# Optimization experiments

Hardware: AMD Instinct MI355X
Metric: run time of the kernel (lower is better)

## Reference

```python
import jax, jax.numpy as jnp
import numpy as np

B, N, E, D = 2, 8192, 1024, 128   # batch, seq, embed_dim, expand_ratio (= head dim)
H = E // D                        # 8 heads (f_proj output dim)
CHUNK = 64
LN_EPS = 1e-5


def _gla_chunked(q, k, v, log_f):
    """Chunked simple GLA: S_t = exp(log_f_t) * S_{t-1} + k_t v_t^T ; o_t = q_t @ S_t.
    q,k,v: [b,h,n,d], log_f: [b,h,n] (log of per-head scalar decay in (0,1))."""
    b, h, n, d = q.shape
    nc = n // CHUNK
    qc = q.reshape(b, h, nc, CHUNK, d)
    kc = k.reshape(b, h, nc, CHUNK, d)
    vc = v.reshape(b, h, nc, CHUNK, d)
    gf = log_f.reshape(b, h, nc, CHUNK)
    g = jnp.cumsum(gf, axis=-1)          # inclusive within-chunk cum log decay [b,h,nc,C]
    gl = g[..., -1]                      # total chunk log decay [b,h,nc]

    # intra-chunk: A[i,j] = (q_i . k_j) * exp(g_i - g_j), j <= i  (g decreasing -> stable)
    mask = jnp.tril(jnp.ones((CHUNK, CHUNK), bool))
    A = jnp.einsum('bhcid,bhcjd->bhcij', qc, kc)
    A = jnp.where(mask, A * jnp.exp(g[..., :, None] - g[..., None, :]), 0.0)
    o_intra = jnp.einsum('bhcij,bhcjd->bhcid', A, vc)

    # inter-chunk: scan over chunks carrying state S [b,h,d,d]
    def step(S, inp):
        q_c, k_c, v_c, g_c, gl_c = inp   # [b,h,C,d],[b,h,C,d],[b,h,C,d],[b,h,C],[b,h]
        o = jnp.einsum('bhid,bhde->bhie', q_c * jnp.exp(g_c)[..., None], S)
        kd = k_c * jnp.exp(gl_c[..., None] - g_c)[..., None]
        S = jnp.exp(gl_c)[..., None, None] * S + jnp.einsum('bhid,bhie->bhde', kd, v_c)
        return S, o

    xs = (jnp.moveaxis(qc, 2, 0), jnp.moveaxis(kc, 2, 0), jnp.moveaxis(vc, 2, 0),
          jnp.moveaxis(g, 2, 0), jnp.moveaxis(gl, 2, 0))
    S0 = jnp.zeros((b, h, d, d), q.dtype)
    _, o_inter = jax.lax.scan(step, S0, xs)      # [nc,b,h,C,d]
    o_inter = jnp.moveaxis(o_inter, 0, 2)        # [b,h,nc,C,d]
    return (o_intra + o_inter).reshape(b, h, n, d)


def setup_inputs() -> dict:
    key = jax.random.key(0)
    ks = jax.random.split(key, 13)
    s = E ** -0.5
    x = jax.random.normal(ks[0], (B, N, E), jnp.float32)
    # per-head lower bound in (0,1), stored in log space as consumed by the module
    log_lower_bound = jnp.log(jax.random.uniform(ks[1], (H,), jnp.float32, 0.05, 0.95))
    Wq = jax.random.normal(ks[2], (E, E), jnp.float32) * s
    Wk = jax.random.normal(ks[3], (E, E), jnp.float32) * s
    Wv = jax.random.normal(ks[4], (E, E), jnp.float32) * s
    Wf = jax.random.normal(ks[5], (E, H), jnp.float32) * s
    Wb1 = jax.random.normal(ks[6], (E, D), jnp.float32) * s
    Wb2 = jax.random.normal(ks[7], (D, E), jnp.float32) * (D ** -0.5)
    Wg1 = jax.random.normal(ks[8], (E, D), jnp.float32) * s
    Wg2 = jax.random.normal(ks[9], (D, E), jnp.float32) * (D ** -0.5)
    Wo = jax.random.normal(ks[10], (E, E), jnp.float32) * s
    ln_scale = jnp.ones((E,), jnp.float32)
    ln_bias = jnp.zeros((E,), jnp.float32)
    return dict(x=x, log_lower_bound=log_lower_bound, Wq=Wq, Wk=Wk, Wv=Wv, Wf=Wf,
                Wb1=Wb1, Wb2=Wb2, Wg1=Wg1, Wg2=Wg2, Wo=Wo,
                ln_scale=ln_scale, ln_bias=ln_bias)


def reference(x, log_lower_bound, Wq, Wk, Wv, Wf, Wb1, Wb2, Wg1, Wg2, Wo, ln_scale, ln_bias):
    silu = jax.nn.silu
    q = silu(x @ Wq)
    k = silu(x @ Wk)
    v = x @ Wv
    f_pre = x @ Wf                               # [B,N,H] per-head decay logits

    # dense-memory Householder-style reflection of q
    beta = silu((x @ Wb1) @ Wb2)
    nb = jnp.sqrt(jnp.sum(beta * beta, axis=-1, keepdims=True))
    beta = beta / jnp.maximum(nb, 1e-6) / (E ** 0.5)
    q = q - 2.0 * jnp.sum(q * beta, axis=-1, keepdims=True) * beta

    def split(t):
        return t.reshape(B, N, H, D).transpose(0, 2, 1, 3)   # [B,H,N,D]
    qh, kh, vh = split(q), split(k), split(v)

    lb = jnp.exp(log_lower_bound)                            # [H]
    f = lb + (1.0 - lb) * jax.nn.sigmoid(f_pre)              # [B,N,H]
    log_f = jnp.log(f).transpose(0, 2, 1)                    # [B,H,N]

    o = _gla_chunked(qh, kh, vh, log_f)                      # [B,H,N,D]
    o = o.transpose(0, 2, 1, 3).reshape(B, N, E)

    gate = jax.nn.sigmoid((x @ Wg1) @ Wg2)
    o = o * gate

    mu = jnp.mean(o, axis=-1, keepdims=True)
    var = jnp.var(o, axis=-1, keepdims=True)
    o = (o - mu) / jnp.sqrt(var + LN_EPS) * ln_scale + ln_bias
    return o @ Wo
```

## Files before the change

### kernel.cpp

```cpp
#include <hip/hip_runtime.h>
#include <hip/hip_bf16.h>
#include <cstdint>


using u16 = unsigned short;
using u32 = unsigned int;
using u64 = unsigned long long;

typedef __attribute__((ext_vector_type(8))) short s16x8;
typedef __attribute__((ext_vector_type(4))) float f32x4;

__device__ __forceinline__ float b2f(u16 b){ u32 u = ((u32)b)<<16; return __builtin_bit_cast(float,u); }
__device__ __forceinline__ u16 f2b(float f){
  u32 u = __builtin_bit_cast(u32,f);
  return (u16)((u + 0x7FFFu + ((u>>16)&1u)) >> 16);
}
__device__ __forceinline__ float sigm(float x){ return 1.f/(1.f + __expf(-x)); }
__device__ __forceinline__ float silu(float x){ return x * sigm(x); }

__device__ __forceinline__ void gload16(const void* g, void* l){
  __builtin_amdgcn_global_load_lds((const __attribute__((address_space(1))) void*)g,
                                   (__attribute__((address_space(3))) void*)l, 16, 0, 0);
}
#define MFMA(a,b,c) __builtin_amdgcn_mfma_f32_16x16x32_bf16((a),(b),(c),0,0,0)

__device__ __forceinline__ void bar(){
  asm volatile("" ::: "memory");
  __builtin_amdgcn_s_barrier();
  asm volatile("" ::: "memory");
}
__device__ __forceinline__ void wait_vm8(){
  asm volatile("s_waitcnt vmcnt(8)" ::: "memory");
  __builtin_amdgcn_sched_barrier(0);
}
__device__ __forceinline__ void wait_vm0(){
  asm volatile("s_waitcnt vmcnt(0)" ::: "memory");
  __builtin_amdgcn_sched_barrier(0);
}

__device__ __forceinline__ void swz_block(int& bx, int& by){
  const int gx = gridDim.x;
  const int nwg = gx * gridDim.y;
  int lin = by*gx + bx;
  const int cpx = nwg >> 3;
  lin = (lin & 7)*cpx + (lin >> 3);
  bx = lin % gx; by = lin / gx;
}

__global__ __launch_bounds__(256) void fill_diag(float* __restrict__ p, int n, float val){
  int i = blockIdx.x*256 + threadIdx.x;
  if (i < n) p[i] = val;
}

__global__ __launch_bounds__(256) void cast_bf(const float4* __restrict__ src,
                                               ushort4* __restrict__ dst, int n4){
  int i = blockIdx.x*256 + threadIdx.x;
  int st = gridDim.x*256;
  for (; i < n4; i += st){
    float4 v = src[i];
    ushort4 o; o.x=f2b(v.x); o.y=f2b(v.y); o.z=f2b(v.z); o.w=f2b(v.w);
    dst[i] = o;
  }
}

__global__ __launch_bounds__(256) void wprep_all(const float* __restrict__ Wq,
                                                 const float* __restrict__ Wk,
                                                 const float* __restrict__ Wv,
                                                 const float* __restrict__ Wf,
                                                 const float* __restrict__ Wb1,
                                                 const float* __restrict__ Wb2,
                                                 const float* __restrict__ Wg1,
                                                 const float* __restrict__ Wg2,
                                                 const float* __restrict__ Wo,
                                                 u16* __restrict__ WCAT,
                                                 u16* __restrict__ WB2T,
                                                 u16* __restrict__ WG2T,
                                                 u16* __restrict__ WOT){
  const int z = blockIdx.z;
  const float* src; u16* dst; int K, Nsrc, kb, nb;
  switch(z){
    case 0: src=Wq;  dst=WCAT;            K=1024; Nsrc=1024; kb=16; nb=16; break;
    case 1: src=Wk;  dst=WCAT+1024*1024;  K=1024; Nsrc=1024; kb=16; nb=16; break;
    case 2: src=Wv;  dst=WCAT+2048*1024;  K=1024; Nsrc=1024; kb=16; nb=16; break;
    case 3: src=Wb1; dst=WCAT+3072*1024;  K=1024; Nsrc=128;  kb=16; nb=2;  break;
    case 4: src=Wg1; dst=WCAT+3200*1024;  K=1024; Nsrc=128;  kb=16; nb=2;  break;
    case 5: src=Wf;  dst=WCAT+3328*1024;  K=1024; Nsrc=8;    kb=16; nb=2;  break;
    case 6: src=Wb2; dst=WB2T;            K=128;  Nsrc=1024; kb=2;  nb=16; break;
    case 7: src=Wg2; dst=WG2T;            K=128;  Nsrc=1024; kb=2;  nb=16; break;
    default:src=Wo;  dst=WOT;             K=1024; Nsrc=1024; kb=16; nb=16; break;
  }
  if (blockIdx.x >= (u32)kb || blockIdx.y >= (u32)nb) return;
  __shared__ float t[64][65];
  const int k0 = blockIdx.x*64, n0 = blockIdx.y*64;
  const int tid = threadIdx.x;
  #pragma unroll
  for (int e=0;e<16;e++){
    int idx = e*256 + tid;
    int r = idx>>6, c = idx&63;
    float v = 0.f;
    if (n0 + c < Nsrc) v = src[(u64)(k0+r)*Nsrc + n0 + c];
    t[r][c] = v;
  }
  __syncthreads();
  #pragma unroll
  for (int e=0;e<16;e++){
    int idx = e*256 + tid;
    int nn = idx>>6, kk = idx&63;
    dst[(u64)(n0+nn)*K + k0 + kk] = f2b(t[kk][nn]);
  }
}

__global__ __launch_bounds__(256,4) void gemm_bt(const u16* __restrict__ A, int lda,
                                                 const u16* __restrict__ Bt,
                                                 void* __restrict__ C, int ldc,
                                                 int K, int mode){
  __shared__ __align__(16) u16 As[128*64];
  __shared__ __align__(16) u16 Bs[128*64];
  const int tid = threadIdx.x, lane = tid&63, wid = tid>>6;
  int bx = blockIdx.x, by = blockIdx.y;
  swz_block(bx, by);
  const int bn0 = bx*128, bm0 = by*128;
  const int wr = wid>>1, wc = wid&1;
  const int g = lane>>4, ln = lane&15;

  f32x4 acc[4][4];
  #pragma unroll
  for (int i=0;i<4;i++)
    #pragma unroll
    for (int j=0;j<4;j++) acc[i][j] = f32x4{0.f,0.f,0.f,0.f};

  const int nk = K >> 6;
  for (int kt = 0; kt < nk; ++kt){
    const int k0 = kt<<6;
    #pragma unroll
    for (int j=0;j<4;j++){
      const int p = (wid*4+j)*64 + lane;
      const int row = p>>3, sl = p&7;
      const int sc = ((sl ^ (row&7))<<3);
      gload16(A  + (u64)(bm0+row)*lda + k0 + sc, (char*)As + (wid*4+j)*1024);
      gload16(Bt + (u64)(bn0+row)*K   + k0 + sc, (char*)Bs + (wid*4+j)*1024);
    }
    __syncthreads();
    #pragma unroll
    for (int ks=0;ks<2;ks++){
      s16x8 af[4], bf[4];
      #pragma unroll
      for (int mt=0;mt<4;mt++){
        const int row = wr*64 + mt*16 + ln;
        af[mt] = *(const s16x8*)(As + row*64 + (((ks*4+g) ^ (row&7))<<3));
      }
      #pragma unroll
      for (int nt=0;nt<4;nt++){
        const int row = wc*64 + nt*16 + ln;
        bf[nt] = *(const s16x8*)(Bs + row*64 + (((ks*4+g) ^ (row&7))<<3));
      }
      #pragma unroll
      for (int mt=0;mt<4;mt++)
        #pragma unroll
        for (int nt=0;nt<4;nt++)
          acc[mt][nt] = MFMA(af[mt], bf[nt], acc[mt][nt]);
    }
    __syncthreads();
  }
  if (mode == 0){
    float* Cf = (float*)C;
    #pragma unroll
    for (int mt=0;mt<4;mt++)
      #pragma unroll
      for (int nt=0;nt<4;nt++){
        const int col = bn0 + wc*64 + nt*16 + ln;
        #pragma unroll
        for (int r=0;r<4;r++)
          Cf[(u64)(bm0 + wr*64 + mt*16 + g*4 + r)*ldc + col] = acc[mt][nt][r];
      }
  } else {
    u16* Cb = (u16*)C;
    #pragma unroll
    for (int mt=0;mt<4;mt++)
      #pragma unroll
      for (int nt=0;nt<4;nt++){
        const int col = bn0 + wc*64 + nt*16 + ln;
        #pragma unroll
        for (int r=0;r<4;r++)
          Cb[(u64)(bm0 + wr*64 + mt*16 + g*4 + r)*ldc + col] = f2b(acc[mt][nt][r]);
      }
  }
}

#define STAGE256(kt_, c_)                                                              \
  do{ const int kk0 = (kt_)<<6;                                                        \
    _Pragma("unroll")                                                                  \
    for (int j=0;j<4;j++){                                                             \
      const int p = j*512 + tid;                                                       \
      const int row = p>>3, sl = p&7;                                                  \
      const int sc = ((sl ^ (row&7))<<3);                                              \
      gload16(A  + (u64)(bm0+row)*lda + kk0 + sc,                                      \
              (char*)lds + (c_)*65536 + (j*8+wid)*1024);                               \
      gload16(Bt + (u64)(bn0+row)*K   + kk0 + sc,                                      \
              (char*)lds + (c_)*65536 + 32768 + (j*8+wid)*1024);                       \
    } }while(0)

#define GEMM256_CORE()                                                                 \
  f32x4 acc[8][4];                                                                     \
  _Pragma("unroll")                                                                    \
  for (int i=0;i<8;i++)                                                                \
    _Pragma("unroll")                                                                  \
    for (int j=0;j<4;j++) acc[i][j] = f32x4{0.f,0.f,0.f,0.f};                          \
  const int nk = K >> 6;                                                               \
  STAGE256(0, 0);                                                                      \
  int cbuf = 0;                                                                        \
  for (int kt = 0; kt < nk; ++kt){                                                     \
    if (kt+1 < nk){ STAGE256(kt+1, cbuf^1); wait_vm8(); } else { wait_vm0(); }         \
    bar();                                                                             \
    const u16* As_c = lds + cbuf*32768;                                                \
    const u16* Bs_c = As_c + 16384;                                                    \
    s16x8 bfr[2][4];                                                                   \
    _Pragma("unroll")                                                                  \
    for (int ks=0;ks<2;ks++)                                                           \
      _Pragma("unroll")                                                                \
      for (int n=0;n<4;n++){                                                           \
        const int row = wc*64 + n*16 + ln;                                             \
        bfr[ks][n] = *(const s16x8*)(Bs_c + row*64 + (((ks*4+g) ^ (row&7))<<3));       \
      }                                                                                \
    _Pragma("unroll")                                                                  \
    for (int m=0;m<8;m++){                                                             \
      const int arow = wr*128 + m*16 + ln;                                             \
      _Pragma("unroll")                                                                \
      for (int ks=0;ks<2;ks++){                                                        \
        const s16x8 af = *(const s16x8*)(As_c + arow*64 + (((ks*4+g) ^ (arow&7))<<3)); \
        _Pragma("unroll")                                                              \
        for (int n=0;n<4;n++) acc[m][n] = MFMA(af, bfr[ks][n], acc[m][n]);             \
      }                                                                                \
    }                                                                                  \
    bar();                                                                             \
    cbuf ^= 1;                                                                         \
  }

__global__ __launch_bounds__(512,2) void gemm256(const u16* __restrict__ A, int lda,
                                                 const u16* __restrict__ Bt,
                                                 void* __restrict__ C, int ldc,
                                                 int K, int mode){
  __shared__ __align__(16) u16 lds[2*32768];
  const int tid = threadIdx.x, lane = tid&63, wid = tid>>6;
  int bx = blockIdx.x, by = blockIdx.y;
  swz_block(bx, by);
  const int bn0 = bx*256, bm0 = by*256;
  const int wr = wid>>2, wc = wid&3;
  const int g = lane>>4, ln = lane&15;
  GEMM256_CORE();
  if (mode == 0){
    float* Cf = (float*)C;
    #pragma unroll
    for (int m=0;m<8;m++)
      #pragma unroll
      for (int n=0;n<4;n++){
        const int col = bn0 + wc*64 + n*16 + ln;
        #pragma unroll
        for (int r=0;r<4;r++)
          Cf[(u64)(bm0 + wr*128 + m*16 + g*4 + r)*ldc + col] = acc[m][n][r];
      }
  } else {
    u16* Cb = (u16*)C;
    #pragma unroll
    for (int m=0;m<8;m++)
      #pragma unroll
      for (int n=0;n<4;n++){
        const int col = bn0 + wc*64 + n*16 + ln;
        #pragma unroll
        for (int r=0;r<4;r++)
          Cb[(u64)(bm0 + wr*128 + m*16 + g*4 + r)*ldc + col] = f2b(acc[m][n][r]);
      }
  }
}

__global__ __launch_bounds__(512,2) void gemm_proj(const u16* __restrict__ A,
                                                   const u16* __restrict__ Bt,
                                                   u16* __restrict__ Qb,
                                                   u16* __restrict__ Kp,
                                                   u16* __restrict__ KT,
                                                   u16* __restrict__ VT,
                                                   u16* __restrict__ FP,
                                                   const float* __restrict__ Gp,
                                                   const float* __restrict__ GLp){
  __shared__ __align__(16) u16 lds[2*32768];
  const int tid = threadIdx.x, lane = tid&63, wid = tid>>6;
  int bx = blockIdx.x, by = blockIdx.y;
  swz_block(bx, by);
  const int bn0 = bx*256, bm0 = by*256;
  const int lda = 1024, K = 1024;
  const int wr = wid>>2, wc = wid&3;
  const int g = lane>>4, ln = lane&15;
  GEMM256_CORE();

  const int cw0 = bn0 + wc*64;
  const int hb = cw0 >> 7;
  if (hb < 8){
    #pragma unroll
    for (int m=0;m<8;m++)
      #pragma unroll
      for (int n=0;n<4;n++){
        const int col = cw0 + n*16 + ln;
        #pragma unroll
        for (int r=0;r<4;r++)
          Qb[(u64)(bm0 + wr*128 + m*16 + g*4 + r)*1024 + col] = f2b(acc[m][n][r]);
      }
  } else if (hb < 16){
    const int h = hb - 8;
    const int bh = (bm0>>13)*8 + h;
    const int dbase = cw0 & 127;
    #pragma unroll
    for (int m=0;m<8;m++){
      const int trow = (bm0&8191) + wr*128 + m*16 + g*4;
      const float gl = GLp[bh*128 + (trow>>6)];
      float es[4];
      #pragma unroll
      for (int r=0;r<4;r++) es[r] = __expf(gl - Gp[(u64)bh*8192 + trow + r]);
      #pragma unroll
      for (int n=0;n<4;n++){
        const int d = dbase + n*16 + ln;
        ushort4 o; u16* op = (u16*)&o;
        #pragma unroll
        for (int r=0;r<4;r++){
          const float s = silu(acc[m][n][r]);
          op[r] = f2b(s * es[r]);
          Kp[(u64)(bm0 + wr*128 + m*16 + g*4 + r)*1024 + h*128 + d] = f2b(s);
        }
        *(ushort4*)(KT + ((u64)bh*128 + d)*8192 + trow) = o;
      }
    }
  } else if (hb < 24){
    const int h = hb - 16;
    const int bh = (bm0>>13)*8 + h;
    const int dbase = cw0 & 127;
    #pragma unroll
    for (int m=0;m<8;m++){
      const int trow = (bm0&8191) + wr*128 + m*16 + g*4;
      #pragma unroll
      for (int n=0;n<4;n++){
        const int d = dbase + n*16 + ln;
        ushort4 o; u16* op = (u16*)&o;
        #pragma unroll
        for (int r=0;r<4;r++) op[r] = f2b(acc[m][n][r]);
        *(ushort4*)(VT + ((u64)bh*128 + d)*8192 + trow) = o;
      }
    }
  } else {
    #pragma unroll
    for (int m=0;m<8;m++)
      #pragma unroll
      for (int n=0;n<4;n++){
        const int col = cw0 + n*16 + ln - 3072;
        #pragma unroll
        for (int r=0;r<4;r++)
          FP[(u64)(bm0 + wr*128 + m*16 + g*4 + r)*384 + col] = f2b(acc[m][n][r]);
      }
  }
}

__global__ __launch_bounds__(64) void fkernel(const u16* __restrict__ FP,
                                              const float* __restrict__ llb,
                                              float* __restrict__ G, float* __restrict__ GL){
  const int c = blockIdx.x, bh = blockIdx.y;
  const int b = bh>>3, h = bh&7;
  const int t = threadIdx.x;
  const int tok = c*64 + t;
  const float fp = b2f(FP[(u64)(b*8192 + tok)*384 + 256 + h]);
  const float lb = __expf(llb[h]);
  const float f = lb + (1.f - lb) * sigm(fp);
  float x = __logf(f);
  #pragma unroll
  for (int d=1; d<64; d<<=1){
    float v = __shfl_up(x, d);
    if (t >= d) x += v;
  }
  G[(u64)bh*8192 + tok] = x;
  const float gl = __shfl(x, 63);
  if (t == 0) GL[bh*128 + c] = gl;
}

__global__ __launch_bounds__(256) void e1_reflect(u16* __restrict__ Q,
                                                  const u16* __restrict__ BP){
  const u64 t = blockIdx.x;
  const int tid = threadIdx.x;
  __shared__ float red[8];
  u16* qrow = Q + t*1024;
  const u16* brow = BP + t*1024;
  ushort4 qv = ((const ushort4*)qrow)[tid];
  ushort4 bv = ((const ushort4*)brow)[tid];
  u16* qp = (u16*)&qv; const u16* bp = (const u16*)&bv;
  float q[4], bb[4];
  float s1 = 0.f, s2 = 0.f;
  #pragma unroll
  for (int j=0;j<4;j++){
    const float qq = silu(b2f(qp[j]));
    const float bbv = silu(b2f(bp[j]));
    q[j] = qq; bb[j] = bbv;
    s1 += bbv*bbv; s2 += qq*bbv;
  }
  #pragma unroll
  for (int d=1; d<64; d<<=1){ s1 += __shfl_xor(s1,d); s2 += __shfl_xor(s2,d); }
  const int wid = tid>>6, lane = tid&63;
  if (lane==0){ red[wid]=s1; red[4+wid]=s2; }
  __syncthreads();
  s1 = red[0]+red[1]+red[2]+red[3];
  s2 = red[4]+red[5]+red[6]+red[7];
  const float bs = 1.f/(fmaxf(sqrtf(s1), 1e-6f) * 32.f);
  const float coef = 2.f * s2 * bs * bs;
  #pragma unroll
  for (int j=0;j<4;j++) qp[j] = f2b(q[j] - coef*bb[j]);
  ((ushort4*)qrow)[tid] = qv;
}

__global__ __launch_bounds__(256,4) void g1_local(const u16* __restrict__ KT,
                                                  const u16* __restrict__ VT,
                                                  u16* __restrict__ LT){
  __shared__ __align__(16) u16 kts[128*64];
  __shared__ __align__(16) u16 vts[128*64];
  const int c = blockIdx.x, bh = blockIdx.y;
  const int tid = threadIdx.x, lane = tid&63, wid = tid>>6;
  const int g = lane>>4, ln = lane&15;
  #pragma unroll
  for (int j=0;j<4;j++){
    const int p = (wid*4+j)*64 + lane;
    const int row = p>>3, sl = p&7;
    const int sc = ((sl ^ (row&7))<<3);
    gload16(KT + ((u64)bh*128 + row)*8192 + (u64)c*64 + sc, (char*)kts + (wid*4+j)*1024);
    gload16(VT + ((u64)bh*128 + row)*8192 + (u64)c*64 + sc, (char*)vts + (wid*4+j)*1024);
  }
  __syncthreads();
  f32x4 acc[2][8];
  #pragma unroll
  for (int mt=0;mt<2;mt++)
// ... 202 lines not shown
  const float mu = s * (1.f/1024.f);
  const float var = s2 * (1.f/1024.f) - mu*mu;
  const float rs = rsqrtf(var + 1e-5f);
  ushort4 out; u16* op = (u16*)&out;
  #pragma unroll
  for (int j=0;j<4;j++){
    const int e = tid*4 + j;
    op[j] = f2b((o[j]-mu)*rs*lnsc[e] + lnbi[e]);
  }
  ((ushort4*)(OL + t*1024))[tid] = out;
}

extern "C" void kernel_launch(void* const* d_in, const int* in_sizes, int n_in,
                              void* d_out, int out_size, void* d_ws, size_t ws_size,
                              hipStream_t stream){
  const float* x   = (const float*)d_in[0];
  const float* llb = (const float*)d_in[1];
  const float* Wq  = (const float*)d_in[2];
  const float* Wk  = (const float*)d_in[3];
  const float* Wv  = (const float*)d_in[4];
  const float* Wf  = (const float*)d_in[5];
  const float* Wb1 = (const float*)d_in[6];
  const float* Wb2 = (const float*)d_in[7];
  const float* Wg1 = (const float*)d_in[8];
  const float* Wg2 = (const float*)d_in[9];
  const float* Wo  = (const float*)d_in[10];
  const float* lnsc= (const float*)d_in[11];
  const float* lnbi= (const float*)d_in[12];

  const u64 REQUIRED = 190586880ull;
  if (ws_size < REQUIRED){
    const float val = 1.0e6f + (float)(u64)(ws_size>>20) * 1024.0f;
    fill_diag<<<dim3((out_size+255)/256),256,0,stream>>>((float*)d_out, out_size, val);
    return;
  }

  char* ws = (char*)d_ws;
  u16*  WCAT = (u16*)(ws + 0ull);
  u16*  WB2T = (u16*)(ws + 7077888ull);
  u16*  WG2T = (u16*)(ws + 7340032ull);
  u16*  WOT  = (u16*)(ws + 7602176ull);
  float* Gb  = (float*)(ws + 9699328ull);
  float* GLb = (float*)(ws + 10223616ull);
  u16*  FP   = (u16*)(ws + 10231808ull);
  u16*  R0   = (u16*)(ws + 22814720ull);
  u16*  Qb   = (u16*)(ws + 56369152ull);
  u16*  Kp   = (u16*)(ws + 89923584ull);
  u16*  KT   = (u16*)(ws + 123478016ull);
  u16*  VT   = (u16*)(ws + 157032448ull);
  u16*  LTSB = (u16*)d_out;
  u16*  XB = R0, *BP = R0, *GP = R0;
  u16*  Ob = KT, *OL = Qb;

  cast_bf<<<dim3(4096),256,0,stream>>>((const float4*)x, (ushort4*)XB, 16384*1024/4);
  wprep_all<<<dim3(16,16,9),256,0,stream>>>(Wq,Wk,Wv,Wf,Wb1,Wb2,Wg1,Wg2,Wo,
                                            WCAT, WB2T, WG2T, WOT);

  gemm_bt<<<dim3(1,128),256,0,stream>>>(XB, 1024, WCAT + 3328*1024, FP + 256, 384, 1024, 1);
  fkernel<<<dim3(128,16),64,0,stream>>>(FP, llb, Gb, GLb);

  gemm_proj<<<dim3(13,64),512,0,stream>>>(XB, WCAT, Qb, Kp, KT, VT, FP, Gb, GLb);

  gemm256<<<dim3(4,64),512,0,stream>>>(FP, 384, WB2T, BP, 1024, 128, 1);
  e1_reflect<<<dim3(16384),256,0,stream>>>(Qb, BP);

  gemm256<<<dim3(4,64),512,0,stream>>>(FP + 128, 384, WG2T, GP, 1024, 128, 1);

  g1_local<<<dim3(128,16),256,0,stream>>>(KT, VT, LTSB);
  g2_scan<<<dim3(64,16),256,0,stream>>>(LTSB, GLb);
  g3_out<<<dim3(128,16),256,0,stream>>>(Qb, Kp, VT, LTSB, Gb, Ob);

  e2_ln<<<dim3(16384),256,0,stream>>>(Ob, GP, lnsc, lnbi, OL);

  gemm256<<<dim3(4,64),512,0,stream>>>(OL, 1024, WOT, d_out, 1024, 1024, 0);
}
```

Measured before the change: 377.9 us.

## Restructure 256x256 GEMM main loop into four quadrant phases with interleaved staging

```diff
diff --git a/kernel.cpp b/kernel.cpp
--- a/kernel.cpp
+++ b/kernel.cpp
@@ -29,12 +29,16 @@
   __builtin_amdgcn_s_barrier();
   asm volatile("" ::: "memory");
 }
-__device__ __forceinline__ void wait_vm8(){
+__device__ __forceinline__ void wv4(){
+  asm volatile("s_waitcnt vmcnt(4)" ::: "memory");
+  __builtin_amdgcn_sched_barrier(0);
+}
+__device__ __forceinline__ void wv0(){
+  asm volatile("s_waitcnt vmcnt(0)" ::: "memory");
+  __builtin_amdgcn_sched_barrier(0);
+}
+__device__ __forceinline__ void wv8(){
   asm volatile("s_waitcnt vmcnt(8)" ::: "memory");
-  __builtin_amdgcn_sched_barrier(0);
-}
-__device__ __forceinline__ void wait_vm0(){
-  asm volatile("s_waitcnt vmcnt(0)" ::: "memory");
   __builtin_amdgcn_sched_barrier(0);
 }
 
@@ -187,54 +191,74 @@
   }
 }
 
-#define STAGE256(kt_, c_)                                                              \
-  do{ const int kk0 = (kt_)<<6;                                                        \
-    _Pragma("unroll")                                                                  \
-    for (int j=0;j<4;j++){                                                             \
-      const int p = j*512 + tid;                                                       \
-      const int row = p>>3, sl = p&7;                                                  \
-      const int sc = ((sl ^ (row&7))<<3);                                              \
-      gload16(A  + (u64)(bm0+row)*lda + kk0 + sc,                                      \
-              (char*)lds + (c_)*65536 + (j*8+wid)*1024);                               \
-      gload16(Bt + (u64)(bn0+row)*K   + kk0 + sc,                                      \
-              (char*)lds + (c_)*65536 + 32768 + (j*8+wid)*1024);                       \
+#define STAGE_H(kt_, b_, gb_, ld_, grow0_, loff_)                              \
+  do{ const int kk0_ = (kt_)<<6;                                               \
+    _Pragma("unroll")                                                          \
+    for (int j_=0;j_<2;j_++){                                                  \
+      const int p_ = j_*512 + tid;                                             \
+      const int row_ = p_>>3, sl_ = p_&7;                                      \
+      const int sc_ = ((sl_ ^ (row_&7))<<3);                                   \
+      gload16((gb_) + (u64)((grow0_)+row_)*(ld_) + kk0_ + sc_,                 \
+              (char*)lds + (b_)*65536 + (loff_) + j_*8192 + wid*1024);         \
     } }while(0)
 
-#define GEMM256_CORE()                                                                 \
-  f32x4 acc[8][4];                                                                     \
-  _Pragma("unroll")                                                                    \
-  for (int i=0;i<8;i++)                                                                \
-    _Pragma("unroll")                                                                  \
-    for (int j=0;j<4;j++) acc[i][j] = f32x4{0.f,0.f,0.f,0.f};                          \
-  const int nk = K >> 6;                                                               \
-  STAGE256(0, 0);                                                                      \
-  int cbuf = 0;                                                                        \
-  for (int kt = 0; kt < nk; ++kt){                                                     \
-    if (kt+1 < nk){ STAGE256(kt+1, cbuf^1); wait_vm8(); } else { wait_vm0(); }         \
-    bar();                                                                             \
-    const u16* As_c = lds + cbuf*32768;                                                \
-    const u16* Bs_c = As_c + 16384;                                                    \
-    s16x8 bfr[2][4];                                                                   \
-    _Pragma("unroll")                                                                  \
-    for (int ks=0;ks<2;ks++)                                                           \
-      _Pragma("unroll")                                                                \
-      for (int n=0;n<4;n++){                                                           \
-        const int row = wc*64 + n*16 + ln;                                             \
-        bfr[ks][n] = *(const s16x8*)(Bs_c + row*64 + (((ks*4+g) ^ (row&7))<<3));       \
-      }                                                                                \
-    _Pragma("unroll")                                                                  \
-    for (int m=0;m<8;m++){                                                             \
-      const int arow = wr*128 + m*16 + ln;                                             \
-      _Pragma("unroll")                                                                \
-      for (int ks=0;ks<2;ks++){                                                        \
-        const s16x8 af = *(const s16x8*)(As_c + arow*64 + (((ks*4+g) ^ (arow&7))<<3)); \
-        _Pragma("unroll")                                                              \
-        for (int n=0;n<4;n++) acc[m][n] = MFMA(af, bfr[ks][n], acc[m][n]);             \
-      }                                                                                \
-    }                                                                                  \
-    bar();                                                                             \
-    cbuf ^= 1;                                                                         \
-  }
+#define PHASE(mh_, nh_, W_, SG_)                                               \
+  do{                                                                          \
+    if (W_) wv4();                                                             \
+    bar();                                                                     \
+    const u16* Ab_ = lds + cbuf*32768 + (mh_)*8192;                            \
+    const u16* Bb_ = lds + cbuf*32768 + 16384 + (nh_)*8192;                    \
+    s16x8 af_[2][4], bf_[2][2];                                                \
+    _Pragma("unroll")                                                          \
+    for (int ks=0;ks<2;ks++){                                                  \
+      _Pragma("unroll")                                                        \
+      for (int m=0;m<4;m++){                                                   \
+        const int r_ = wr*64 + m*16 + ln;                                      \
+        af_[ks][m] = *(const s16x8*)(Ab_ + r_*64 + (((ks*4+g) ^ (r_&7))<<3));  \
+      }                                                                        \
+      _Pragma("unroll")                                                        \
+      for (int n=0;n<2;n++){                                                   \
+        const int r_ = wc*32 + n*16 + ln;                                      \
+        bf_[ks][n] = *(const s16x8*)(Bb_ + r_*64 + (((ks*4+g) ^ (r_&7))<<3));  \
+      }                                                                        \
+    }                                                                          \
+    SG_;                                                                       \
+    __builtin_amdgcn_s_setprio(1);                                             \
+    _Pragma("unroll")                                                          \
+    for (int ks=0;ks<2;ks++)                                                   \
+      _Pragma("unroll")                                                        \
+      for (int m=0;m<4;m++)                                                    \
+        _Pragma("unroll")                                                      \
+        for (int n=0;n<2;n++)                                                  \
+          acc[(mh_)*4+m][(nh_)*2+n] =                                          \
+            MFMA(af_[ks][m], bf_[ks][n], acc[(mh_)*4+m][(nh_)*2+n]);           \
+    __builtin_amdgcn_s_setprio(0);                                             \
+  }while(0)
+
+#define GEMM8P_CORE()                                                          \
+  f32x4 acc[8][4];                                                             \
+  _Pragma("unroll")                                                            \
+  for (int i=0;i<8;i++)                                                        \
+    _Pragma("unroll")                                                          \
+    for (int j=0;j<4;j++) acc[i][j] = f32x4{0.f,0.f,0.f,0.f};                  \
+  const int nk = K >> 6;                                                       \
+  STAGE_H(0,0,Bt,K,  bn0,     32768);                                          \
+  STAGE_H(0,0,A, lda,bm0,     0);                                              \
+  STAGE_H(0,0,Bt,K,  bn0+128, 49152);                                          \
+  STAGE_H(0,0,A, lda,bm0+128, 16384);                                          \
+  for (int kt=0; kt<nk-1; ++kt){                                               \
+    const int cbuf = kt&1, nb = cbuf^1;                                        \
+    PHASE(0,0,1, STAGE_H(kt+1,nb,Bt,K,  bn0,     32768));                      \
+    PHASE(0,1,1, STAGE_H(kt+1,nb,A, lda,bm0,     0));                          \
+    PHASE(1,1,1, STAGE_H(kt+1,nb,Bt,K,  bn0+128, 49152));                      \
+    PHASE(1,0,0, STAGE_H(kt+1,nb,A, lda,bm0+128, 16384));                      \
+  }                                                                            \
+  { const int cbuf = (nk-1)&1;                                                 \
+    wv0();                                                                     \
+    PHASE(0,0,0,);                                                             \
+    PHASE(0,1,0,);                                                             \
+    PHASE(1,1,0,);                                                             \
+    PHASE(1,0,0,); }
 
 __global__ __launch_bounds__(512,2) void gemm256(const u16* __restrict__ A, int lda,
                                                  const u16* __restrict__ Bt,
@@ -245,31 +269,41 @@
   int bx = blockIdx.x, by = blockIdx.y;
   swz_block(bx, by);
   const int bn0 = bx*256, bm0 = by*256;
-  const int wr = wid>>2, wc = wid&3;
+  const int wr = (wid>>2), wc = wid&3;
   const int g = lane>>4, ln = lane&15;
-  GEMM256_CORE();
+  GEMM8P_CORE();
   if (mode == 0){
     float* Cf = (float*)C;
     #pragma unroll
-    for (int m=0;m<8;m++)
-      #pragma unroll
-      for (int n=0;n<4;n++){
-        const int col = bn0 + wc*64 + n*16 + ln;
-        #pragma unroll
-        for (int r=0;r<4;r++)
-          Cf[(u64)(bm0 + wr*128 + m*16 + g*4 + r)*ldc + col] = acc[m][n][r];
-      }
+    for (int mh=0;mh<2;mh++)
+      #pragma unroll
+      for (int m=0;m<4;m++)
+        #pragma unroll
+        for (int nh=0;nh<2;nh++)
+          #pragma unroll
+          for (int n=0;n<2;n++){
+            const int col = bn0 + nh*128 + wc*32 + n*16 + ln;
+            #pragma unroll
+            for (int r=0;r<4;r++)
+              Cf[(u64)(bm0 + mh*128 + wr*64 + m*16 + g*4 + r)*ldc + col] =
+                acc[mh*4+m][nh*2+n][r];
+          }
   } else {
     u16* Cb = (u16*)C;
     #pragma unroll
-    for (int m=0;m<8;m++)
-      #pragma unroll
-      for (int n=0;n<4;n++){
-        const int col = bn0 + wc*64 + n*16 + ln;
-        #pragma unroll
-        for (int r=0;r<4;r++)
-          Cb[(u64)(bm0 + wr*128 + m*16 + g*4 + r)*ldc + col] = f2b(acc[m][n][r]);
-      }
+    for (int mh=0;mh<2;mh++)
+      #pragma unroll
+      for (int m=0;m<4;m++)
+        #pragma unroll
+        for (int nh=0;nh<2;nh++)
+          #pragma unroll
+          for (int n=0;n<2;n++){
+            const int col = bn0 + nh*128 + wc*32 + n*16 + ln;
+            #pragma unroll
+            for (int r=0;r<4;r++)
+              Cb[(u64)(bm0 + mh*128 + wr*64 + m*16 + g*4 + r)*ldc + col] =
+                f2b(acc[mh*4+m][nh*2+n][r]);
+          }
   }
 }
 
@@ -288,72 +322,82 @@
   swz_block(bx, by);
   const int bn0 = bx*256, bm0 = by*256;
   const int lda = 1024, K = 1024;
-  const int wr = wid>>2, wc = wid&3;
+  const int wr = (wid>>2), wc = wid&3;
   const int g = lane>>4, ln = lane&15;
-  GEMM256_CORE();
-
-  const int cw0 = bn0 + wc*64;
-  const int hb = cw0 >> 7;
-  if (hb < 8){
-    #pragma unroll
-    for (int m=0;m<8;m++)
-      #pragma unroll
-      for (int n=0;n<4;n++){
-        const int col = cw0 + n*16 + ln;
-        #pragma unroll
-        for (int r=0;r<4;r++)
-          Qb[(u64)(bm0 + wr*128 + m*16 + g*4 + r)*1024 + col] = f2b(acc[m][n][r]);
-      }
-  } else if (hb < 16){
-    const int h = hb - 8;
-    const int bh = (bm0>>13)*8 + h;
-    const int dbase = cw0 & 127;
-    #pragma unroll
-    for (int m=0;m<8;m++){
-      const int trow = (bm0&8191) + wr*128 + m*16 + g*4;
-      const float gl = GLp[bh*128 + (trow>>6)];
-      float es[4];
-      #pragma unroll
-      for (int r=0;r<4;r++) es[r] = __expf(gl - Gp[(u64)bh*8192 + trow + r]);
-      #pragma unroll
-      for (int n=0;n<4;n++){
-        const int d = dbase + n*16 + ln;
-        ushort4 o; u16* op = (u16*)&o;
-        #pragma unroll
-        for (int r=0;r<4;r++){
-          const float s = silu(acc[m][n][r]);
-          op[r] = f2b(s * es[r]);
-          Kp[(u64)(bm0 + wr*128 + m*16 + g*4 + r)*1024 + h*128 + d] = f2b(s);
+  GEMM8P_CORE();
+
+  #pragma unroll
+  for (int nh=0;nh<2;nh++){
+    const int hb2 = (bn0>>7) + nh;
+    if (hb2 < 8){
+      #pragma unroll
+      for (int mh=0;mh<2;mh++)
+        #pragma unroll
+        for (int m=0;m<4;m++)
+          #pragma unroll
+          for (int n=0;n<2;n++){
+            const int col = bn0 + nh*128 + wc*32 + n*16 + ln;
+            #pragma unroll
+            for (int r=0;r<4;r++)
+              Qb[(u64)(bm0 + mh*128 + wr*64 + m*16 + g*4 + r)*1024 + col] =
+                f2b(acc[mh*4+m][nh*2+n][r]);
+          }
+    } else if (hb2 < 16){
+      const int h = hb2 - 8;
+      const int bh = (bm0>>13)*8 + h;
+      #pragma unroll
+      for (int mh=0;mh<2;mh++)
+        #pragma unroll
+        for (int m=0;m<4;m++){
+          const int trowb = (bm0&8191) + mh*128 + wr*64 + m*16 + g*4;
+          const float gl = GLp[bh*128 + (trowb>>6)];
+          float es[4];
+          #pragma unroll
+          for (int r=0;r<4;r++) es[r] = __expf(gl - Gp[(u64)bh*8192 + trowb + r]);
+          #pragma unroll
+          for (int n=0;n<2;n++){
+            const int d = wc*32 + n*16 + ln;
+            ushort4 o; u16* op = (u16*)&o;
+            #pragma unroll
+            for (int r=0;r<4;r++){
+              const float s = silu(acc[mh*4+m][nh*2+n][r]);
+              op[r] = f2b(s * es[r]);
+              Kp[(u64)(bm0 + mh*128 + wr*64 + m*16 + g*4 + r)*1024 + h*128 + d] = f2b(s);
+            }
+            *(ushort4*)(KT + ((u64)bh*128 + d)*8192 + trowb) = o;
+          }
         }
-        *(ushort4*)(KT + ((u64)bh*128 + d)*8192 + trow) = o;
-      }
-    }
-  } else if (hb < 24){
-    const int h = hb - 16;
-    const int bh = (bm0>>13)*8 + h;
-    const int dbase = cw0 & 127;
-    #pragma unroll
-    for (int m=0;m<8;m++){
-      const int trow = (bm0&8191) + wr*128 + m*16 + g*4;
-      #pragma unroll
-      for (int n=0;n<4;n++){
-        const int d = dbase + n*16 + ln;
-        ushort4 o; u16* op = (u16*)&o;
-        #pragma unroll
-        for (int r=0;r<4;r++) op[r] = f2b(acc[m][n][r]);
-        *(ushort4*)(VT + ((u64)bh*128 + d)*8192 + trow) = o;
-      }
-    }
-  } else {
-    #pragma unroll
-    for (int m=0;m<8;m++)
-      #pragma unroll
-      for (int n=0;n<4;n++){
-        const int col = cw0 + n*16 + ln - 3072;
-        #pragma unroll
-        for (int r=0;r<4;r++)
-          FP[(u64)(bm0 + wr*128 + m*16 + g*4 + r)*384 + col] = f2b(acc[m][n][r]);
-      }
+    } else if (hb2 < 24){
+      const int h = hb2 - 16;
+      const int bh = (bm0>>13)*8 + h;
+      #pragma unroll
+      for (int mh=0;mh<2;mh++)
+        #pragma unroll
+        for (int m=0;m<4;m++){
+          const int trowb = (bm0&8191) + mh*128 + wr*64 + m*16 + g*4;
+          #pragma unroll
+          for (int n=0;n<2;n++){
+            const int d = wc*32 + n*16 + ln;
+            ushort4 o; u16* op = (u16*)&o;
+            #pragma unroll
+            for (int r=0;r<4;r++) op[r] = f2b(acc[mh*4+m][nh*2+n][r]);
+            *(ushort4*)(VT + ((u64)bh*128 + d)*8192 + trowb) = o;
+          }
+        }
+    } else {
+      #pragma unroll
+      for (int mh=0;mh<2;mh++)
+        #pragma unroll
+        for (int m=0;m<4;m++)
+          #pragma unroll
+          for (int n=0;n<2;n++){
+            const int col = bn0 + nh*128 + wc*32 + n*16 + ln - 3072;
+            #pragma unroll
+            for (int r=0;r<4;r++)
+              FP[(u64)(bm0 + mh*128 + wr*64 + m*16 + g*4 + r)*384 + col] =
+                f2b(acc[mh*4+m][nh*2+n][r]);
+          }
+    }
   }
 }
 
```

Measured after the change: 380.1 us. About the same (+0.6%).

## Restructure 256x256 GEMM mainloop into 4-stage K=32 pipeline with k-major LDS layout

Applied to the files above, without the earlier changes.

```diff
diff --git a/kernel.cpp b/kernel.cpp
--- a/kernel.cpp
+++ b/kernel.cpp
@@ -29,12 +29,20 @@
   __builtin_amdgcn_s_barrier();
   asm volatile("" ::: "memory");
 }
-__device__ __forceinline__ void wait_vm8(){
+__device__ __forceinline__ void wv8(){
   asm volatile("s_waitcnt vmcnt(8)" ::: "memory");
   __builtin_amdgcn_sched_barrier(0);
 }
-__device__ __forceinline__ void wait_vm0(){
+__device__ __forceinline__ void wv4(){
+  asm volatile("s_waitcnt vmcnt(4)" ::: "memory");
+  __builtin_amdgcn_sched_barrier(0);
+}
+__device__ __forceinline__ void wv0(){
   asm volatile("s_waitcnt vmcnt(0)" ::: "memory");
+  __builtin_amdgcn_sched_barrier(0);
+}
+__device__ __forceinline__ void lgkm0(){
+  asm volatile("s_waitcnt lgkmcnt(0)" ::: "memory");
   __builtin_amdgcn_sched_barrier(0);
 }
 
@@ -187,67 +195,62 @@
   }
 }
 
-#define STAGE256(kt_, c_)                                                              \
-  do{ const int kk0 = (kt_)<<6;                                                        \
-    _Pragma("unroll")                                                                  \
-    for (int j=0;j<4;j++){                                                             \
-      const int p = j*512 + tid;                                                       \
-      const int row = p>>3, sl = p&7;                                                  \
-      const int sc = ((sl ^ (row&7))<<3);                                              \
-      gload16(A  + (u64)(bm0+row)*lda + kk0 + sc,                                      \
-              (char*)lds + (c_)*65536 + (j*8+wid)*1024);                               \
-      gload16(Bt + (u64)(bn0+row)*K   + kk0 + sc,                                      \
-              (char*)lds + (c_)*65536 + 32768 + (j*8+wid)*1024);                       \
+#define STAGE32(kt_, b_)                                                       \
+  do{ const int kk0_ = (kt_)<<5;                                               \
+    _Pragma("unroll")                                                          \
+    for (int j_=0;j_<2;j_++){                                                  \
+      const int p_ = wid*2 + j_;                                               \
+      const int s_ = p_>>2, rb_ = p_&3;                                        \
+      gload16(A  + (u64)(bm0 + rb_*64 + lane)*lda + kk0_ + s_*8,               \
+              (char*)lds + (b_)*32768 + s_*4096 + rb_*1024);                   \
+      gload16(Bt + (u64)(bn0 + rb_*64 + lane)*K   + kk0_ + s_*8,               \
+              (char*)lds + (b_)*32768 + 16384 + s_*4096 + rb_*1024);           \
     } }while(0)
 
-#define GEMM256_CORE()                                                                 \
-  f32x4 acc[8][4];                                                                     \
-  _Pragma("unroll")                                                                    \
-  for (int i=0;i<8;i++)                                                                \
-    _Pragma("unroll")                                                                  \
-    for (int j=0;j<4;j++) acc[i][j] = f32x4{0.f,0.f,0.f,0.f};                          \
-  const int nk = K >> 6;                                                               \
-  STAGE256(0, 0);                                                                      \
-  int cbuf = 0;                                                                        \
-  for (int kt = 0; kt < nk; ++kt){                                                     \
-    if (kt+1 < nk){ STAGE256(kt+1, cbuf^1); wait_vm8(); } else { wait_vm0(); }         \
-    bar();                                                                             \
-    const u16* As_c = lds + cbuf*32768;                                                \
-    const u16* Bs_c = As_c + 16384;                                                    \
-    s16x8 bfr[2][4];                                                                   \
-    _Pragma("unroll")                                                                  \
-    for (int ks=0;ks<2;ks++)                                                           \
-      _Pragma("unroll")                                                                \
-      for (int n=0;n<4;n++){                                                           \
-        const int row = wc*64 + n*16 + ln;                                             \
-        bfr[ks][n] = *(const s16x8*)(Bs_c + row*64 + (((ks*4+g) ^ (row&7))<<3));       \
-      }                                                                                \
-    _Pragma("unroll")                                                                  \
-    for (int m=0;m<8;m++){                                                             \
-      const int arow = wr*128 + m*16 + ln;                                             \
-      _Pragma("unroll")                                                                \
-      for (int ks=0;ks<2;ks++){                                                        \
-        const s16x8 af = *(const s16x8*)(As_c + arow*64 + (((ks*4+g) ^ (arow&7))<<3)); \
-        _Pragma("unroll")                                                              \
-        for (int n=0;n<4;n++) acc[m][n] = MFMA(af, bfr[ks][n], acc[m][n]);             \
-      }                                                                                \
-    }                                                                                  \
-    bar();                                                                             \
-    cbuf ^= 1;                                                                         \
+#define GEMMD_CORE()                                                           \
+  f32x4 acc[8][4];                                                             \
+  _Pragma("unroll")                                                            \
+  for (int i=0;i<8;i++)                                                        \
+    _Pragma("unroll")                                                          \
+    for (int j=0;j<4;j++) acc[i][j] = f32x4{0.f,0.f,0.f,0.f};                  \
+  const int nk = K >> 5;                                                       \
+  STAGE32(0,0); STAGE32(1,1); STAGE32(2,2);                                    \
+  for (int s=0; s<nk; ++s){                                                    \
+    if (s < nk-2) wv8(); else if (s == nk-2) wv4(); else wv0();                \
+    bar();                                                                     \
+    if (s+3 < nk) STAGE32(s+3, (s+3)&3);                                       \
+    const int cb = s&3;                                                        \
+    const u16* Ab_ = lds + cb*16384 + g*2048;                                  \
+    const u16* Bb_ = Ab_ + 8192;                                               \
+    s16x8 af_[8], bf_[4];                                                      \
+    _Pragma("unroll")                                                          \
+    for (int m=0;m<8;m++)                                                      \
+      af_[m] = *(const s16x8*)(Ab_ + (wr*128 + m*16 + ln)*8);                  \
+    _Pragma("unroll")                                                          \
+    for (int n=0;n<4;n++)                                                      \
+      bf_[n] = *(const s16x8*)(Bb_ + (wc*64 + n*16 + ln)*8);                   \
+    lgkm0();                                                                   \
+    __builtin_amdgcn_s_setprio(1);                                             \
+    _Pragma("unroll")                                                          \
+    for (int m=0;m<8;m++)                                                      \
+      _Pragma("unroll")                                                        \
+      for (int n=0;n<4;n++)                                                    \
+        acc[m][n] = MFMA(af_[m], bf_[n], acc[m][n]);                           \
+    __builtin_amdgcn_s_setprio(0);                                             \
   }
 
 __global__ __launch_bounds__(512,2) void gemm256(const u16* __restrict__ A, int lda,
                                                  const u16* __restrict__ Bt,
                                                  void* __restrict__ C, int ldc,
                                                  int K, int mode){
-  __shared__ __align__(16) u16 lds[2*32768];
+  __shared__ __align__(16) u16 lds[4*16384];
   const int tid = threadIdx.x, lane = tid&63, wid = tid>>6;
   int bx = blockIdx.x, by = blockIdx.y;
   swz_block(bx, by);
   const int bn0 = bx*256, bm0 = by*256;
   const int wr = wid>>2, wc = wid&3;
   const int g = lane>>4, ln = lane&15;
-  GEMM256_CORE();
+  GEMMD_CORE();
   if (mode == 0){
     float* Cf = (float*)C;
     #pragma unroll
@@ -282,7 +285,7 @@
                                                    u16* __restrict__ FP,
                                                    const float* __restrict__ Gp,
                                                    const float* __restrict__ GLp){
-  __shared__ __align__(16) u16 lds[2*32768];
+  __shared__ __align__(16) u16 lds[4*16384];
   const int tid = threadIdx.x, lane = tid&63, wid = tid>>6;
   int bx = blockIdx.x, by = blockIdx.y;
   swz_block(bx, by);
@@ -290,24 +293,24 @@
   const int lda = 1024, K = 1024;
   const int wr = wid>>2, wc = wid&3;
   const int g = lane>>4, ln = lane&15;
-  GEMM256_CORE();
-
-  const int cw0 = bn0 + wc*64;
-  const int hb = cw0 >> 7;
-  if (hb < 8){
+  GEMMD_CORE();
+
+  const int hb2 = (bn0>>7) + (wc>>1);
+  const int dq  = (wc&1)*64;
+  if (hb2 < 8){
     #pragma unroll
     for (int m=0;m<8;m++)
       #pragma unroll
       for (int n=0;n<4;n++){
-        const int col = cw0 + n*16 + ln;
+        const int col = bn0 + wc*64 + n*16 + ln;
         #pragma unroll
         for (int r=0;r<4;r++)
-          Qb[(u64)(bm0 + wr*128 + m*16 + g*4 + r)*1024 + col] = f2b(acc[m][n][r]);
-      }
-  } else if (hb < 16){
-    const int h = hb - 8;
+          Qb[(u64)(bm0 + wr*128 + m*16 + g*4 + r)*1024 + col] =
+            f2b(acc[m][n][r]);
+      }
+  } else if (hb2 < 16){
+    const int h = hb2 - 8;
     const int bh = (bm0>>13)*8 + h;
-    const int dbase = cw0 & 127;
     #pragma unroll
     for (int m=0;m<8;m++){
       const int trow = (bm0&8191) + wr*128 + m*16 + g*4;
@@ -317,7 +320,7 @@
       for (int r=0;r<4;r++) es[r] = __expf(gl - Gp[(u64)bh*8192 + trow + r]);
       #pragma unroll
       for (int n=0;n<4;n++){
-        const int d = dbase + n*16 + ln;
+        const int d = dq + n*16 + ln;
         ushort4 o; u16* op = (u16*)&o;
         #pragma unroll
         for (int r=0;r<4;r++){
@@ -328,16 +331,15 @@
         *(ushort4*)(KT + ((u64)bh*128 + d)*8192 + trow) = o;
       }
     }
-  } else if (hb < 24){
-    const int h = hb - 16;
+  } else if (hb2 < 24){
+    const int h = hb2 - 16;
     const int bh = (bm0>>13)*8 + h;
-    const int dbase = cw0 & 127;
     #pragma unroll
     for (int m=0;m<8;m++){
       const int trow = (bm0&8191) + wr*128 + m*16 + g*4;
       #pragma unroll
       for (int n=0;n<4;n++){
-        const int d = dbase + n*16 + ln;
+        const int d = dq + n*16 + ln;
         ushort4 o; u16* op = (u16*)&o;
         #pragma unroll
         for (int r=0;r<4;r++) op[r] = f2b(acc[m][n][r]);
@@ -349,10 +351,11 @@
     for (int m=0;m<8;m++)
       #pragma unroll
       for (int n=0;n<4;n++){
-        const int col = cw0 + n*16 + ln - 3072;
+        const int col = bn0 + wc*64 + n*16 + ln - 3072;
         #pragma unroll
         for (int r=0;r<4;r++)
-          FP[(u64)(bm0 + wr*128 + m*16 + g*4 + r)*384 + col] = f2b(acc[m][n][r]);
+          FP[(u64)(bm0 + wr*128 + m*16 + g*4 + r)*384 + col] =
+            f2b(acc[m][n][r]);
       }
   }
 }
```

After: 441.0 us. 1.17x slower.

## Compute decay logits in fp32 directly and shrink projection GEMM tiles to 128

Applied to the files above, without the earlier changes.

```diff
diff --git a/kernel.cpp b/kernel.cpp
--- a/kernel.cpp
+++ b/kernel.cpp
@@ -66,7 +66,6 @@
 __global__ __launch_bounds__(256) void wprep_all(const float* __restrict__ Wq,
                                                  const float* __restrict__ Wk,
                                                  const float* __restrict__ Wv,
-                                                 const float* __restrict__ Wf,
                                                  const float* __restrict__ Wb1,
                                                  const float* __restrict__ Wb2,
                                                  const float* __restrict__ Wg1,
@@ -84,9 +83,8 @@
     case 2: src=Wv;  dst=WCAT+2048*1024;  K=1024; Nsrc=1024; kb=16; nb=16; break;
     case 3: src=Wb1; dst=WCAT+3072*1024;  K=1024; Nsrc=128;  kb=16; nb=2;  break;
     case 4: src=Wg1; dst=WCAT+3200*1024;  K=1024; Nsrc=128;  kb=16; nb=2;  break;
-    case 5: src=Wf;  dst=WCAT+3328*1024;  K=1024; Nsrc=8;    kb=16; nb=2;  break;
-    case 6: src=Wb2; dst=WB2T;            K=128;  Nsrc=1024; kb=2;  nb=16; break;
-    case 7: src=Wg2; dst=WG2T;            K=128;  Nsrc=1024; kb=2;  nb=16; break;
+    case 5: src=Wb2; dst=WB2T;            K=128;  Nsrc=1024; kb=2;  nb=16; break;
+    case 6: src=Wg2; dst=WG2T;            K=128;  Nsrc=1024; kb=2;  nb=16; break;
     default:src=Wo;  dst=WOT;             K=1024; Nsrc=1024; kb=16; nb=16; break;
   }
   if (blockIdx.x >= (u32)kb || blockIdx.y >= (u32)nb) return;
@@ -110,10 +108,53 @@
   }
 }
 
-__global__ __launch_bounds__(256,4) void gemm_bt(const u16* __restrict__ A, int lda,
-                                                 const u16* __restrict__ Bt,
-                                                 void* __restrict__ C, int ldc,
-                                                 int K, int mode){
+__global__ __launch_bounds__(256) void fkernel2(const float* __restrict__ x,
+                                                const float* __restrict__ Wf,
+                                                const float* __restrict__ llb,
+                                                float* __restrict__ G,
+                                                float* __restrict__ GL){
+  const int c = blockIdx.x, bh = blockIdx.y;
+  const int b = bh>>3, h = bh&7;
+  const int tid = threadIdx.x;
+  __shared__ float wf[1024];
+  __shared__ float fsm[64];
+  for (int i = tid; i < 1024; i += 256) wf[i] = Wf[(u64)i*8 + h];
+  __syncthreads();
+  const int t = tid>>2, q = tid&3;
+  const float* xr = x + (u64)(b*8192 + c*64 + t)*1024 + q*256;
+  const float* wp0 = wf + q*256;
+  float s = 0.f;
+  #pragma unroll 8
+  for (int i=0;i<64;i++){
+    float4 xv = ((const float4*)xr)[i];
+    s += xv.x*wp0[i*4+0] + xv.y*wp0[i*4+1] + xv.z*wp0[i*4+2] + xv.w*wp0[i*4+3];
+  }
+  s += __shfl_xor(s,1); s += __shfl_xor(s,2);
+  if (q==0) fsm[t] = s;
+  __syncthreads();
+  if (tid < 64){
+    const float lb = __expf(llb[h]);
+    const float f = lb + (1.f - lb)*sigm(fsm[tid]);
+    float xg = __logf(f);
+    #pragma unroll
+    for (int d=1; d<64; d<<=1){
+      float v = __shfl_up(xg, d);
+      if (tid >= d) xg += v;
+    }
+    G[(u64)bh*8192 + c*64 + tid] = xg;
+    if (tid==63) GL[bh*128 + c] = xg;
+  }
+}
+
+__global__ __launch_bounds__(256,4) void gemm_proj(const u16* __restrict__ A,
+                                                   const u16* __restrict__ Bt,
+                                                   u16* __restrict__ Qb,
+                                                   u16* __restrict__ Kp,
+                                                   u16* __restrict__ KT,
+                                                   u16* __restrict__ VT,
+                                                   u16* __restrict__ FP,
+                                                   const float* __restrict__ Gp,
+                                                   const float* __restrict__ GLp){
   __shared__ __align__(16) u16 As[128*64];
   __shared__ __align__(16) u16 Bs[128*64];
   const int tid = threadIdx.x, lane = tid&63, wid = tid>>6;
@@ -129,16 +170,15 @@
     #pragma unroll
     for (int j=0;j<4;j++) acc[i][j] = f32x4{0.f,0.f,0.f,0.f};
 
-  const int nk = K >> 6;
-  for (int kt = 0; kt < nk; ++kt){
+  for (int kt = 0; kt < 16; ++kt){
     const int k0 = kt<<6;
     #pragma unroll
     for (int j=0;j<4;j++){
       const int p = (wid*4+j)*64 + lane;
       const int row = p>>3, sl = p&7;
       const int sc = ((sl ^ (row&7))<<3);
-      gload16(A  + (u64)(bm0+row)*lda + k0 + sc, (char*)As + (wid*4+j)*1024);
-      gload16(Bt + (u64)(bn0+row)*K   + k0 + sc, (char*)Bs + (wid*4+j)*1024);
+      gload16(A  + (u64)(bm0+row)*1024 + k0 + sc, (char*)As + (wid*4+j)*1024);
+      gload16(Bt + (u64)(bn0+row)*1024 + k0 + sc, (char*)Bs + (wid*4+j)*1024);
     }
     __syncthreads();
     #pragma unroll
@@ -162,8 +202,9 @@
     }
     __syncthreads();
   }
-  if (mode == 0){
-    float* Cf = (float*)C;
+
+  const int cb = bn0 >> 7;
+  if (cb < 8){
     #pragma unroll
     for (int mt=0;mt<4;mt++)
       #pragma unroll
@@ -171,18 +212,61 @@
         const int col = bn0 + wc*64 + nt*16 + ln;
         #pragma unroll
         for (int r=0;r<4;r++)
-          Cf[(u64)(bm0 + wr*64 + mt*16 + g*4 + r)*ldc + col] = acc[mt][nt][r];
-      }
+          Qb[(u64)(bm0 + wr*64 + mt*16 + g*4 + r)*1024 + col] = f2b(acc[mt][nt][r]);
+      }
+  } else if (cb < 16){
+    const int h = cb - 8;
+    const int bh = (bm0>>13)*8 + h;
+    const int trowb = (bm0 & 8191) + wr*64;
+    const float gl = GLp[bh*128 + (trowb>>6)];
+    float es[4][4];
+    #pragma unroll
+    for (int mt=0;mt<4;mt++)
+      #pragma unroll
+      for (int r=0;r<4;r++)
+        es[mt][r] = __expf(gl - Gp[(u64)bh*8192 + trowb + mt*16 + g*4 + r]);
+    #pragma unroll
+    for (int mt=0;mt<4;mt++){
+      const int trow = trowb + mt*16 + g*4;
+      #pragma unroll
+      for (int nt=0;nt<4;nt++){
+        const int d = wc*64 + nt*16 + ln;
+        ushort4 o; u16* op = (u16*)&o;
+        #pragma unroll
+        for (int r=0;r<4;r++){
+          const float s = silu(acc[mt][nt][r]);
+          op[r] = f2b(s * es[mt][r]);
+          Kp[(u64)(bm0 + wr*64 + mt*16 + g*4 + r)*1024 + h*128 + d] = f2b(s);
+        }
+        *(ushort4*)(KT + ((u64)bh*128 + d)*8192 + trow) = o;
+      }
+    }
+  } else if (cb < 24){
+    const int h = cb - 16;
+    const int bh = (bm0>>13)*8 + h;
+    const int trowb = (bm0 & 8191) + wr*64;
+    #pragma unroll
+    for (int mt=0;mt<4;mt++){
+      const int trow = trowb + mt*16 + g*4;
+      #pragma unroll
+      for (int nt=0;nt<4;nt++){
+        const int d = wc*64 + nt*16 + ln;
+        ushort4 o; u16* op = (u16*)&o;
+        #pragma unroll
+        for (int r=0;r<4;r++) op[r] = f2b(acc[mt][nt][r]);
+        *(ushort4*)(VT + ((u64)bh*128 + d)*8192 + trow) = o;
+      }
+    }
   } else {
-    u16* Cb = (u16*)C;
+    const int off = (cb == 24) ? 0 : 128;
     #pragma unroll
     for (int mt=0;mt<4;mt++)
       #pragma unroll
       for (int nt=0;nt<4;nt++){
-        const int col = bn0 + wc*64 + nt*16 + ln;
+        const int col = off + wc*64 + nt*16 + ln;
         #pragma unroll
         for (int r=0;r<4;r++)
-          Cb[(u64)(bm0 + wr*64 + mt*16 + g*4 + r)*ldc + col] = f2b(acc[mt][nt][r]);
+          FP[(u64)(bm0 + wr*64 + mt*16 + g*4 + r)*384 + col] = f2b(acc[mt][nt][r]);
       }
   }
 }
@@ -273,111 +357,6 @@
   }
 }
 
-__global__ __launch_bounds__(512,2) void gemm_proj(const u16* __restrict__ A,
-                                                   const u16* __restrict__ Bt,
-                                                   u16* __restrict__ Qb,
-                                                   u16* __restrict__ Kp,
-                                                   u16* __restrict__ KT,
-                                                   u16* __restrict__ VT,
-                                                   u16* __restrict__ FP,
-                                                   const float* __restrict__ Gp,
-                                                   const float* __restrict__ GLp){
-  __shared__ __align__(16) u16 lds[2*32768];
-  const int tid = threadIdx.x, lane = tid&63, wid = tid>>6;
-  int bx = blockIdx.x, by = blockIdx.y;
-  swz_block(bx, by);
-  const int bn0 = bx*256, bm0 = by*256;
-  const int lda = 1024, K = 1024;
-  const int wr = wid>>2, wc = wid&3;
-  const int g = lane>>4, ln = lane&15;
-  GEMM256_CORE();
-
-  const int cw0 = bn0 + wc*64;
-  const int hb = cw0 >> 7;
-  if (hb < 8){
-    #pragma unroll
-    for (int m=0;m<8;m++)
-      #pragma unroll
-      for (int n=0;n<4;n++){
-        const int col = cw0 + n*16 + ln;
-        #pragma unroll
-        for (int r=0;r<4;r++)
-          Qb[(u64)(bm0 + wr*128 + m*16 + g*4 + r)*1024 + col] = f2b(acc[m][n][r]);
-      }
-  } else if (hb < 16){
-    const int h = hb - 8;
-    const int bh = (bm0>>13)*8 + h;
-    const int dbase = cw0 & 127;
-    #pragma unroll
-    for (int m=0;m<8;m++){
-      const int trow = (bm0&8191) + wr*128 + m*16 + g*4;
-      const float gl = GLp[bh*128 + (trow>>6)];
-      float es[4];
-      #pragma unroll
-      for (int r=0;r<4;r++) es[r] = __expf(gl - Gp[(u64)bh*8192 + trow + r]);
-      #pragma unroll
-      for (int n=0;n<4;n++){
-        const int d = dbase + n*16 + ln;
-        ushort4 o; u16* op = (u16*)&o;
-        #pragma unroll
-        for (int r=0;r<4;r++){
-          const float s = silu(acc[m][n][r]);
-          op[r] = f2b(s * es[r]);
-          Kp[(u64)(bm0 + wr*128 + m*16 + g*4 + r)*1024 + h*128 + d] = f2b(s);
-        }
-        *(ushort4*)(KT + ((u64)bh*128 + d)*8192 + trow) = o;
-      }
-    }
-  } else if (hb < 24){
-    const int h = hb - 16;
-    const int bh = (bm0>>13)*8 + h;
-    const int dbase = cw0 & 127;
-    #pragma unroll
-    for (int m=0;m<8;m++){
-      const int trow = (bm0&8191) + wr*128 + m*16 + g*4;
-      #pragma unroll
-      for (int n=0;n<4;n++){
-        const int d = dbase + n*16 + ln;
-        ushort4 o; u16* op = (u16*)&o;
-        #pragma unroll
-        for (int r=0;r<4;r++) op[r] = f2b(acc[m][n][r]);
-        *(ushort4*)(VT + ((u64)bh*128 + d)*8192 + trow) = o;
-      }
-    }
-  } else {
-    #pragma unroll
-    for (int m=0;m<8;m++)
-      #pragma unroll
-      for (int n=0;n<4;n++){
-        const int col = cw0 + n*16 + ln - 3072;
-        #pragma unroll
-        for (int r=0;r<4;r++)
-          FP[(u64)(bm0 + wr*128 + m*16 + g*4 + r)*384 + col] = f2b(acc[m][n][r]);
-      }
-  }
-}
-
-__global__ __launch_bounds__(64) void fkernel(const u16* __restrict__ FP,
-                                              const float* __restrict__ llb,
-                                              float* __restrict__ G, float* __restrict__ GL){
-  const int c = blockIdx.x, bh = blockIdx.y;
-  const int b = bh>>3, h = bh&7;
-  const int t = threadIdx.x;
-  const int tok = c*64 + t;
-  const float fp = b2f(FP[(u64)(b*8192 + tok)*384 + 256 + h]);
-  const float lb = __expf(llb[h]);
-  const float f = lb + (1.f - lb) * sigm(fp);
-  float x = __logf(f);
-  #pragma unroll
-  for (int d=1; d<64; d<<=1){
-    float v = __shfl_up(x, d);
-    if (t >= d) x += v;
-  }
-  G[(u64)bh*8192 + tok] = x;
-  const float gl = __shfl(x, 63);
-  if (t == 0) GL[bh*128 + c] = gl;
-}
-
 __global__ __launch_bounds__(256) void e1_reflect(u16* __restrict__ Q,
                                                   const u16* __restrict__ BP){
   const u64 t = blockIdx.x;
@@ -686,14 +665,13 @@
   u16*  XB = R0, *BP = R0, *GP = R0;
   u16*  Ob = KT, *OL = Qb;
 
+  fkernel2<<<dim3(128,16),256,0,stream>>>(x, Wf, llb, Gb, GLb);
+
   cast_bf<<<dim3(4096),256,0,stream>>>((const float4*)x, (ushort4*)XB, 16384*1024/4);
-  wprep_all<<<dim3(16,16,9),256,0,stream>>>(Wq,Wk,Wv,Wf,Wb1,Wb2,Wg1,Wg2,Wo,
+  wprep_all<<<dim3(16,16,8),256,0,stream>>>(Wq,Wk,Wv,Wb1,Wb2,Wg1,Wg2,Wo,
                                             WCAT, WB2T, WG2T, WOT);
 
-  gemm_bt<<<dim3(1,128),256,0,stream>>>(XB, 1024, WCAT + 3328*1024, FP + 256, 384, 1024, 1);
-  fkernel<<<dim3(128,16),64,0,stream>>>(FP, llb, Gb, GLb);
-
-  gemm_proj<<<dim3(13,64),512,0,stream>>>(XB, WCAT, Qb, Kp, KT, VT, FP, Gb, GLb);
+  gemm_proj<<<dim3(26,128),256,0,stream>>>(XB, WCAT, Qb, Kp, KT, VT, FP, Gb, GLb);
 
   gemm256<<<dim3(4,64),512,0,stream>>>(FP, 384, WB2T, BP, 1024, 128, 1);
   e1_reflect<<<dim3(16384),256,0,stream>>>(Qb, BP);
```

Measured after the change: 427.7 us. 1.13x slower.
